# Kernel tuning notes

Hardware: AMD Instinct MI355X
Metric: run time of the kernel (lower is better)

The kernel has to match this reference:

```python
import jax, jax.numpy as jnp
import numpy as np

N_NODES = 10000
N_EDGES = 320000
NODE_F = 64
EDGE_F = 32
H = 256
L = 6
HEADS = 8
OUT = H // HEADS
N_GRAPHS = 16
NEG_SLOPE = 0.2  # PyG GATConv leaky_relu slope


def setup_inputs() -> dict:
    key = jax.random.key(0)
    ks = jax.random.split(key, 32)
    s = 0.05
    f32 = jnp.float32
    inp = {}
    inp["x"] = jax.random.normal(ks[0], (N_NODES, NODE_F), f32)
    inp["edge_index"] = jax.random.randint(ks[1], (2, N_EDGES), 0, N_NODES)
    inp["edge_attr"] = jax.random.normal(ks[2], (N_EDGES, EDGE_F), f32)
    inp["batch"] = jnp.sort(jax.random.randint(ks[3], (N_NODES,), 0, N_GRAPHS))
    # embeddings
    inp["node_w"] = jax.random.normal(ks[4], (H, NODE_F), f32) * s
    inp["node_b"] = jnp.zeros((H,), f32)
    inp["edge_emb_w"] = jax.random.normal(ks[5], (H, EDGE_F), f32) * s
    inp["edge_emb_b"] = jnp.zeros((H,), f32)
    # stacked GATConv params (shared lin for src/dst since in_channels is int)
    inp["lin_w"] = jax.random.normal(ks[6], (L, H, H), f32) * s
    inp["att_src"] = jax.random.normal(ks[7], (L, HEADS, OUT), f32) * s
    inp["att_dst"] = jax.random.normal(ks[8], (L, HEADS, OUT), f32) * s
    inp["att_edge"] = jax.random.normal(ks[9], (L, HEADS, OUT), f32) * s
    inp["lin_edge_w"] = jax.random.normal(ks[10], (L, H, H), f32) * s
    inp["conv_b"] = jnp.zeros((L, H), f32)
    inp["ln_g"] = jnp.ones((L, H), f32)
    inp["ln_b"] = jnp.zeros((L, H), f32)
    # MLP heads: Linear(2H->H), Linear(H->H/2), Linear(H/2->3)
    inp["pw1"] = jax.random.normal(ks[11], (H, 2 * H), f32) * s
    inp["pb1"] = jnp.zeros((H,), f32)
    inp["pw2"] = jax.random.normal(ks[12], (H // 2, H), f32) * s
    inp["pb2"] = jnp.zeros((H // 2,), f32)
    inp["pw3"] = jax.random.normal(ks[13], (3, H // 2), f32) * s
    inp["pb3"] = jnp.zeros((3,), f32)
    inp["mw1"] = jax.random.normal(ks[14], (H, 2 * H), f32) * s
    inp["mb1"] = jnp.zeros((H,), f32)
    inp["mw2"] = jax.random.normal(ks[15], (H // 2, H), f32) * s
    inp["mb2"] = jnp.zeros((H // 2,), f32)
    inp["mw3"] = jax.random.normal(ks[16], (3, H // 2), f32) * s
    inp["mb3"] = jnp.zeros((3,), f32)
    return inp


def _ln(x, g, b):
    mu = jnp.mean(x, -1, keepdims=True)
    var = jnp.mean(jnp.square(x - mu), -1, keepdims=True)
    return g * (x - mu) * jax.lax.rsqrt(var + 1e-5) + b


def _mlp(z, w1, b1, w2, b2, w3, b3):
    h = jax.nn.gelu(z @ w1.T + b1, approximate=False)
    h = jax.nn.gelu(h @ w2.T + b2, approximate=False)
    return jax.nn.sigmoid(h @ w3.T + b3)


def _gnn_forward(x, edge_attr, src, dst, batch,
                 node_w, node_b, edge_emb_w, edge_emb_b,
                 lin_w, att_src, att_dst, att_edge, lin_edge_w, conv_b,
                 ln_g, ln_b,
                 pw1, pb1, pw2, pb2, pw3, pb3,
                 mw1, mb1, mw2, mb2, mw3, mb3):
    h = x @ node_w.T + node_b                       # [N, H]
    ea = edge_attr @ edge_emb_w.T + edge_emb_b      # [E, H]
    # PyG add_self_loops(fill_value='mean'): loop attr = mean of incoming edge attrs
    cnt = jax.ops.segment_sum(jnp.ones((N_EDGES,), h.dtype), dst, N_NODES)
    loop_attr = jax.ops.segment_sum(ea, dst, N_NODES) / jnp.maximum(cnt, 1.0)[:, None]
    ea_full = jnp.concatenate([ea, loop_attr], 0)   # [E+N, H]
    loops = jnp.arange(N_NODES, dtype=src.dtype)
    src_f = jnp.concatenate([src, loops])
    dst_f = jnp.concatenate([dst, loops])
    for i in range(L):
        x_in = h
        xw = (h @ lin_w[i].T).reshape(N_NODES, HEADS, OUT)
        eap = (ea_full @ lin_edge_w[i].T).reshape(-1, HEADS, OUT)
        a_src = jnp.sum(xw * att_src[i], -1)        # [N, heads]
        a_dst = jnp.sum(xw * att_dst[i], -1)
        alpha = a_src[src_f] + a_dst[dst_f] + jnp.sum(eap * att_edge[i], -1)  # [E+N, heads]
        alpha = jnp.where(alpha > 0, alpha, NEG_SLOPE * alpha)
        amax = jax.ops.segment_max(alpha, dst_f, N_NODES)
        e = jnp.exp(alpha - amax[dst_f])
        denom = jax.ops.segment_sum(e, dst_f, N_NODES)
        w = e / (denom[dst_f] + 1e-16)
        msg = xw[src_f] * w[:, :, None]             # [E+N, heads, out]
        hi = jax.ops.segment_sum(msg, dst_f, N_NODES).reshape(N_NODES, H) + conv_b[i]
        hi = jax.nn.gelu(_ln(hi, ln_g[i], ln_b[i]), approximate=False)
        h = hi + x_in if i > 0 else hi
    sums = jax.ops.segment_sum(h, batch, N_GRAPHS)  # [G, H]
    ncnt = jax.ops.segment_sum(jnp.ones((N_NODES,), h.dtype), batch, N_GRAPHS)
    mean = sums / jnp.maximum(ncnt, 1.0)[:, None]
    xg = jnp.concatenate([mean, sums], 1)           # [G, 2H]
    params = _mlp(xg, pw1, pb1, pw2, pb2, pw3, pb3)
    metrics = _mlp(xg, mw1, mb1, mw2, mb2, mw3, mb3)
    return params, metrics


def reference(x, edge_index, edge_attr, batch,
              node_w, node_b, edge_emb_w, edge_emb_b,
              lin_w, att_src, att_dst, att_edge, lin_edge_w, conv_b,
              ln_g, ln_b,
              pw1, pb1, pw2, pb2, pw3, pb3,
              mw1, mb1, mw2, mb2, mw3, mb3):
    return _gnn_forward(x, edge_attr, edge_index[0], edge_index[1], batch,
                        node_w, node_b, edge_emb_w, edge_emb_b,
                        lin_w, att_src, att_dst, att_edge, lin_edge_w, conv_b,
                        ln_g, ln_b,
                        pw1, pb1, pw2, pb2, pw3, pb3,
                        mw1, mb1, mw2, mb2, mw3, mb3)
```

## Files before the change

### kernel.cpp

```cpp
#include <hip/hip_runtime.h>
#include <math.h>

#define NN 10000
#define NE 320000
#define NODE_F 64
#define EDGE_F 32
#define HDIM 256
#define HEADS 8
#define LAYERS 6
#define NG 16
#define NPB 2
#define NOUT 48
#define LOG2E 1.4426950408889634f

typedef __attribute__((ext_vector_type(8))) short short8;
typedef __attribute__((ext_vector_type(4))) float float4v;
typedef __attribute__((ext_vector_type(2))) float floatx2;

__global__ void count_kernel(const int* __restrict__ dst, int* __restrict__ cnt) {
    int e = blockIdx.x * 256 + threadIdx.x;
    if (e < NE) atomicAdd(&cnt[dst[e]], 1);
}

__global__ void scan_kernel(const int* __restrict__ cnt, int* __restrict__ row_ptr,
                            int* __restrict__ pos) {
    __shared__ int wsum[16];
    __shared__ int woff[16];
    int t = threadIdx.x;
    int lane = t & 63, wid = t >> 6;
    const int chunk = 10;
    int lo = t * chunk;
    int loc[10];
    int s = 0;
    #pragma unroll
    for (int k = 0; k < 10; ++k) {
        int i = lo + k;
        int v = (i < NN) ? cnt[i] : 0;
        loc[k] = v;
        s += v;
    }
    int inc = s;
    #pragma unroll
    for (int off = 1; off < 64; off <<= 1) {
        int v = __shfl_up(inc, off, 64);
        if (lane >= off) inc += v;
    }
    if (lane == 63) wsum[wid] = inc;
    __syncthreads();
    if (t < 16) {
        int inc2 = wsum[t];
        #pragma unroll
        for (int off = 1; off < 16; off <<= 1) {
            int u = __shfl_up(inc2, off, 16);
            if (t >= off) inc2 += u;
        }
        woff[t] = inc2;
    }
    __syncthreads();
    int base = inc - s + (wid ? woff[wid - 1] : 0);
    #pragma unroll
    for (int k = 0; k < 10; ++k) {
        int i = lo + k;
        if (i < NN) {
            row_ptr[i] = base;
            pos[i] = base;
            base += loc[k];
        }
    }
    if (t == 1023) row_ptr[NN] = woff[15];
}

__device__ __forceinline__ ushort f2bf(float f) {
    union { float f; unsigned u; } v; v.f = f;
    unsigned u = v.u;
    return (ushort)((u + 0x7fffu + ((u >> 16) & 1u)) >> 16);
}
__device__ __forceinline__ float bf2f(ushort b) {
    union { unsigned u; float f; } v; v.u = ((unsigned)b) << 16; return v.f;
}

__global__ __launch_bounds__(256) void prep_kernel(const float* __restrict__ att_edge,
                                                   const float* __restrict__ lin_edge_w,
                                                   const float* __restrict__ eew,
                                                   const float* __restrict__ eeb,
                                                   ushort* __restrict__ webbf,
                                                   float* __restrict__ bebuf) {
    int ih = blockIdx.x;
    int i = ih >> 3, h = ih & 7;
    __shared__ float vsh[HDIM];
    int t = threadIdx.x;
    float s = 0.f;
    const float* ae = att_edge + ih * 32;
    const float* lw = lin_edge_w + ((size_t)i * HDIM + h * 32) * HDIM + t;
    #pragma unroll
    for (int o = 0; o < 32; ++o) s += ae[o] * lw[(size_t)o * HDIM];
    vsh[t] = s;
    __syncthreads();
    if (t < EDGE_F) {
        float acc = 0.f;
        for (int k = 0; k < HDIM; ++k) acc += vsh[k] * eew[k * EDGE_F + t];
        webbf[ih * EDGE_F + t] = f2bf(acc * LOG2E);
    } else if (t == EDGE_F) {
        float acc = 0.f;
        for (int k = 0; k < HDIM; ++k) acc += vsh[k] * eeb[k];
        bebuf[ih] = acc * LOG2E;
    }
}

__global__ __launch_bounds__(256) void scatterE_kernel(const int* __restrict__ src,
                                                       const int* __restrict__ dst,
                                                       const float* __restrict__ edge_attr,
                                                       int* __restrict__ pos,
                                                       int* __restrict__ csr_src,
                                                       const ushort* __restrict__ web,
                                                       const float* __restrict__ be,
                                                       ushort* __restrict__ preEb) {
    int wv = threadIdx.x >> 6, l = threadIdx.x & 63;
    int base = blockIdx.x * 64 + wv * 16;
    int m = l & 15, kq = (l >> 4) * 8;
    int idxl = 0;
    if (l < 16) {
        int e = base + l;
        int d = dst[e];
        idxl = atomicAdd(&pos[d], 1);
        csr_src[idxl] = src[e];
    }
    const float* ar = edge_attr + (size_t)(base + m) * EDGE_F + kq;
    float4 a0 = *(const float4*)(ar);
    float4 a1 = *(const float4*)(ar + 4);
    short8 afrag;
    afrag[0] = (short)f2bf(a0.x); afrag[1] = (short)f2bf(a0.y);
    afrag[2] = (short)f2bf(a0.z); afrag[3] = (short)f2bf(a0.w);
    afrag[4] = (short)f2bf(a1.x); afrag[5] = (short)f2bf(a1.y);
    afrag[6] = (short)f2bf(a1.z); afrag[7] = (short)f2bf(a1.w);
    float4v zero = {0.f, 0.f, 0.f, 0.f};
    float4v acc[3];
    #pragma unroll
    for (int ct = 0; ct < 3; ++ct) {
        short8 bfrag = *(const short8*)(web + (size_t)(ct * 16 + m) * EDGE_F + kq);
        acc[ct] = __builtin_amdgcn_mfma_f32_16x16x32_bf16(afrag, bfrag, zero, 0, 0, 0);
    }
    #pragma unroll
    for (int ct = 0; ct < 3; ++ct) {
        int oc = ct * 16 + m;
        int li = oc >> 3, hh = oc & 7;
        float bv = be[oc];
        #pragma unroll
        for (int r = 0; r < 4; ++r) {
            int row = (l >> 4) * 4 + r;
            int ridx = __shfl(idxl, row, 64);
            preEb[(size_t)li * NE * 8 + (size_t)ridx * 8 + hh] = f2bf(acc[ct][r] + bv);
        }
    }
}

__global__ __launch_bounds__(256) void preL_kernel(const ushort* __restrict__ preEb,
                                                   const int* __restrict__ row_ptr,
                                                   float* __restrict__ preL) {
    int g = threadIdx.x >> 5, c = threadIdx.x & 31;
    int n = blockIdx.x * 8 + g;
    int start = row_ptr[n], end = row_ptr[n + 1];
    int deg = end - start;
    float s[NOUT] = {};
    for (int idx = start + c; idx < end; idx += 32) {
        #pragma unroll
        for (int li = 0; li < LAYERS; ++li) {
            uint4 pk = *(const uint4*)(preEb + (size_t)li * NE * 8 + (size_t)idx * 8);
            s[li * 8 + 0] += bf2f((ushort)(pk.x & 0xffff));
            s[li * 8 + 1] += bf2f((ushort)(pk.x >> 16));
            s[li * 8 + 2] += bf2f((ushort)(pk.y & 0xffff));
            s[li * 8 + 3] += bf2f((ushort)(pk.y >> 16));
            s[li * 8 + 4] += bf2f((ushort)(pk.z & 0xffff));
            s[li * 8 + 5] += bf2f((ushort)(pk.z >> 16));
            s[li * 8 + 6] += bf2f((ushort)(pk.w & 0xffff));
            s[li * 8 + 7] += bf2f((ushort)(pk.w >> 16));
        }
    }
    #pragma unroll
    for (int off = 16; off >= 1; off >>= 1)
        #pragma unroll
        for (int h = 0; h < NOUT; ++h) s[h] += __shfl_xor(s[h], off, 32);
    if (c == 0) {
        float invd = deg > 0 ? 1.f / (float)deg : 0.f;
        for (int li = 0; li < LAYERS; ++li) {
            float4* dstp = (float4*)(preL + ((size_t)li * NN + n) * 8);
            dstp[0] = make_float4(s[li * 8 + 0] * invd, s[li * 8 + 1] * invd,
                                  s[li * 8 + 2] * invd, s[li * 8 + 3] * invd);
            dstp[1] = make_float4(s[li * 8 + 4] * invd, s[li * 8 + 5] * invd,
                                  s[li * 8 + 6] * invd, s[li * 8 + 7] * invd);
        }
    }
}

__global__ void tobf_all_kernel(const float* __restrict__ lin_w, const float* __restrict__ node_w,
                                const float* __restrict__ x, ushort* __restrict__ wbhi,
                                ushort* __restrict__ nwhi, ushort* __restrict__ xhi) {
    const int N1 = LAYERS * HDIM * HDIM;
    const int N2 = N1 + HDIM * NODE_F;
    const int N3 = N2 + NN * NODE_F;
    int i = blockIdx.x * 256 + threadIdx.x;
    if (i < N1) wbhi[i] = f2bf(lin_w[i]);
    else if (i < N2) nwhi[i - N1] = f2bf(node_w[i - N1]);
    else if (i < N3) xhi[i - N2] = f2bf(x[i - N2]);
}

__global__ __launch_bounds__(128) void gemm_bf1(const ushort* __restrict__ Ah,
                                                const ushort* __restrict__ Bh,
                                                const float* __restrict__ bias,
                                                float* __restrict__ C,
                                                ushort* __restrict__ Chi,
                                                unsigned char* __restrict__ Cf8,
                                                const float* __restrict__ att_s,
                                                const float* __restrict__ att_d,
                                                float* __restrict__ a_src,
                                                float* __restrict__ a_dst,
                                                int N, int K, int J) {
    __shared__ ushort sAh[64][40], sBh[64][40];
    int nb = blockIdx.y * 64, jb = blockIdx.x * 64;
    int t = threadIdx.x, w = t >> 6, l = t & 63;
    int srow = t >> 1, sq = (t & 1) * 16;
    int fr = l & 15, fq = (l >> 4) * 8;
    float4v acc[2][4] = {};
    for (int kt = 0; kt < K; kt += 32) {
        int gr = nb + srow;
        short8 a0 = {0,0,0,0,0,0,0,0}, a1 = {0,0,0,0,0,0,0,0};
        if (gr < N) {
            const short8* pa = (const short8*)(Ah + (size_t)gr * K + kt + sq);
            a0 = pa[0]; a1 = pa[1];
        }
        *(short8*)&sAh[srow][sq] = a0; *(short8*)&sAh[srow][sq + 8] = a1;
        const short8* pb = (const short8*)(Bh + (size_t)(jb + srow) * K + kt + sq);
        short8 b0 = pb[0], b1 = pb[1];
        *(short8*)&sBh[srow][sq] = b0; *(short8*)&sBh[srow][sq + 8] = b1;
        __syncthreads();
        short8 bh[4];
        #pragma unroll
        for (int nt = 0; nt < 4; ++nt)
            bh[nt] = *(const short8*)&sBh[nt * 16 + fr][fq];
        #pragma unroll
        for (int mt = 0; mt < 2; ++mt) {
            short8 ah = *(const short8*)&sAh[w * 32 + mt * 16 + fr][fq];
            #pragma unroll
            for (int nt = 0; nt < 4; ++nt)
                acc[mt][nt] = __builtin_amdgcn_mfma_f32_16x16x32_bf16(ah, bh[nt], acc[mt][nt], 0, 0, 0);
        }
        __syncthreads();
    }
    #pragma unroll
    for (int mt = 0; mt < 2; ++mt) {
        #pragma unroll
        for (int nt = 0; nt < 4; ++nt) {
            int col = jb + nt * 16 + fr;
            float bv = bias ? bias[col] : 0.f;
            #pragma unroll
            for (int r = 0; r < 4; ++r) {
                int row = nb + w * 32 + mt * 16 + (l >> 4) * 4 + r;
                if (row < N) {
                    float v = acc[mt][nt][r] + bv;
                    if (C) C[(size_t)row * J + col] = v;
                    if (Chi) Chi[(size_t)row * J + col] = f2bf(v);
                    if (Cf8) {
                        int pk8 = __builtin_amdgcn_cvt_pk_fp8_f32(v, v, 0, false);
                        Cf8[(size_t)row * J + col] = (unsigned char)(pk8 & 0xff);
                    }
                }
            }
        }
    }
    if (att_s) {
        int head0 = jb >> 5;
        float cs[4], cd[4];
        #pragma unroll
        for (int nt = 0; nt < 4; ++nt) {
            cs[nt] = att_s[jb + nt * 16 + fr] * LOG2E;
            cd[nt] = att_d[jb + nt * 16 + fr] * LOG2E;
        }
        #pragma unroll
        for (int mt = 0; mt < 2; ++mt) {
            #pragma unroll
            for (int r = 0; r < 4; ++r) {
                float s0 = acc[mt][0][r] * cs[0] + acc[mt][1][r] * cs[1];
                float s1 = acc[mt][2][r] * cs[2] + acc[mt][3][r] * cs[3];
                float d0 = acc[mt][0][r] * cd[0] + acc[mt][1][r] * cd[1];
                float d1 = acc[mt][2][r] * cd[2] + acc[mt][3][r] * cd[3];
                #pragma unroll
                for (int off = 8; off >= 1; off >>= 1) {
                    s0 += __shfl_xor(s0, off, 16);
                    s1 += __shfl_xor(s1, off, 16);
                    d0 += __shfl_xor(d0, off, 16);
                    d1 += __shfl_xor(d1, off, 16);
                }
                if (fr == 0) {
                    int row = nb + w * 32 + mt * 16 + (l >> 4) * 4 + r;
                    if (row < N) {
                        a_src[row * 8 + head0]     = s0;
                        a_src[row * 8 + head0 + 1] = s1;
                        a_dst[row * 8 + head0]     = d0;
                        a_dst[row * 8 + head0 + 1] = d1;
                    }
                }
            }
        }
    }
}

__device__ __forceinline__ float gelu_exact(float x) {
    return 0.5f * x * (1.f + erff(x * 0.70710678118654752f));
}

__global__ __launch_bounds__(64 * NPB) void node_kernel(const unsigned char* __restrict__ xwf8,
                                                  const ushort* __restrict__ pb,
                                                  const float* __restrict__ preL,
                                                  const float* __restrict__ a_src,
                                                  const float* __restrict__ a_dst,
                                                  const int* __restrict__ row_ptr,
                                                  const int* __restrict__ csr_src,
                                                  const float* __restrict__ h_prev,
                                                  float* __restrict__ h_next,
                                                  ushort* __restrict__ hhi,
                                                  const float* __restrict__ cb,
                                                  const float* __restrict__ lg,
                                                  const float* __restrict__ lb, int first) {
    int wv = threadIdx.x >> 6, l = threadIdx.x & 63;
    int n = blockIdx.x * NPB + wv;
    int start = row_ptr[n], end = row_ptr[n + 1];
    int hc = l >> 3;
    int hc8 = l & 56;
    int jj = l & 7;
    float adnh = a_dst[n * 8 + hc];
    const unsigned char* xb = xwf8 + 4 * l;

    float den, acc[4];
    {
        float al = a_src[n * 8 + hc] + adnh + preL[n * 8 + hc];
        al = fminf(fmaxf(al, 0.2f * al), 57.7f);
        float wself = exp2f(al);
        den = wself;
        unsigned gs = *(const unsigned*)(xb + (size_t)n * HDIM);
        floatx2 lo = __builtin_amdgcn_cvt_pk_f32_fp8(gs, false);
        floatx2 hi = __builtin_amdgcn_cvt_pk_f32_fp8(gs, true);
        acc[0] = wself * lo.x;
        acc[1] = wself * lo.y;
        acc[2] = wself * hi.x;
        acc[3] = wself * hi.y;
    }
    int idx = start;
    for (; idx + 8 <= end; idx += 8) {
        int sn[8];
        #pragma unroll
        for (int j = 0; j < 8; ++j) sn[j] = csr_src[idx + j];
        int sn_t = csr_src[idx + jj];
        float p_t = bf2f(pb[(size_t)(idx + jj) * 8 + hc]);
        float a_t = a_src[(size_t)sn_t * 8 + hc] + adnh + p_t;
        float w_t = exp2f(fminf(fmaxf(a_t, 0.2f * a_t), 57.7f));
        unsigned g[8];
        #pragma unroll
        for (int j = 0; j < 8; ++j) g[j] = *(const unsigned*)(xb + (size_t)sn[j] * HDIM);
        #pragma unroll
        for (int j = 0; j < 8; ++j) {
            float wj = __shfl(w_t, hc8 + j, 64);
            floatx2 lo = __builtin_amdgcn_cvt_pk_f32_fp8(g[j], false);
            floatx2 hi = __builtin_amdgcn_cvt_pk_f32_fp8(g[j], true);
            den += wj;
            acc[0] += wj * lo.x;
            acc[1] += wj * lo.y;
            acc[2] += wj * hi.x;
            acc[3] += wj * hi.y;
        }
    }
    for (; idx < end; ++idx) {
        int sn = csr_src[idx];
        unsigned g = *(const unsigned*)(xb + (size_t)sn * HDIM);
        float a = a_src[(size_t)sn * 8 + hc] + adnh + bf2f(pb[(size_t)idx * 8 + hc]);
        float wt = exp2f(fminf(fmaxf(a, 0.2f * a), 57.7f));
        floatx2 lo = __builtin_amdgcn_cvt_pk_f32_fp8(g, false);
        floatx2 hi = __builtin_amdgcn_cvt_pk_f32_fp8(g, true);
        den += wt;
        acc[0] += wt * lo.x;
        acc[1] += wt * lo.y;
        acc[2] += wt * hi.x;
        acc[3] += wt * hi.y;
    }
    float4 cb4 = *(const float4*)(cb + 4 * l);
    float invh = 1.f / (den + 1e-16f);
    acc[0] = acc[0] * invh + cb4.x;
    acc[1] = acc[1] * invh + cb4.y;
    acc[2] = acc[2] * invh + cb4.z;
    acc[3] = acc[3] * invh + cb4.w;

    float part = acc[0] + acc[1] + acc[2] + acc[3];
    #pragma unroll
    for (int off = 32; off >= 1; off >>= 1) part += __shfl_xor(part, off, 64);
    float mu = part * (1.f / 256.f);
    float p2 = 0.f;
    #pragma unroll
    for (int j = 0; j < 4; ++j) {
        float d = acc[j] - mu;
        p2 += d * d;
    }
    #pragma unroll
    for (int off = 32; off >= 1; off >>= 1) p2 += __shfl_xor(p2, off, 64);
    float rstd = rsqrtf(p2 * (1.f / 256.f) + 1e-5f);

    float4 lg4 = *(const float4*)(lg + 4 * l);
    float4 lb4 = *(const float4*)(lb + 4 * l);
    float o4[4];
    float lgv[4] = {lg4.x, lg4.y, lg4.z, lg4.w};
    float lbv[4] = {lb4.x, lb4.y, lb4.z, lb4.w};
    float4 hp = make_float4(0.f, 0.f, 0.f, 0.f);
    if (!first) hp = *(const float4*)(h_prev + (size_t)n * HDIM + 4 * l);
    float hpv[4] = {hp.x, hp.y, hp.z, hp.w};
    #pragma unroll
    for (int j = 0; j < 4; ++j) {
        float y = (acc[j] - mu) * rstd * lgv[j] + lbv[j];
        o4[j] = gelu_exact(y) + hpv[j];
    }
    *(float4*)(h_next + (size_t)n * HDIM + 4 * l) = make_float4(o4[0], o4[1], o4[2], o4[3]);
    if (hhi) {
        uint2 ph;
        ph.x = (unsigned)f2bf(o4[0]) | ((unsigned)f2bf(o4[1]) << 16);
        ph.y = (unsigned)f2bf(o4[2]) | ((unsigned)f2bf(o4[3]) << 16);
        *(uint2*)(hhi + (size_t)n * HDIM + 4 * l) = ph;
    }
}

__global__ __launch_bounds__(256) void graph_sum_kernel(const float* __restrict__ h,
                                                        const int* __restrict__ batch,
                                                        float* __restrict__ sums) {
    int t = threadIdx.x;
    int n0 = blockIdx.x * 64;
    int n1 = min(NN, n0 + 64);
    float acc = 0.f;
    int cur = batch[n0];
    for (int n = n0; n < n1; ++n) {
        int b = batch[n];
        if (b != cur) {
            atomicAdd(&sums[cur * HDIM + t], acc);
            acc = 0.f;
            cur = b;
        }
        acc += h[(size_t)n * HDIM + t];
    }
    atomicAdd(&sums[cur * HDIM + t], acc);
}

__device__ __forceinline__ int lower_bound_dev(const int* a, int n, int v) {
    int lo = 0, hi = n;
    while (lo < hi) {
        int mid = (lo + hi) >> 1;
        if (a[mid] < v) lo = mid + 1; else hi = mid;
    }
    return lo;
}

__global__ __launch_bounds__(256) void mlp_kernel(const float* __restrict__ sums,
                                                  const int* __restrict__ batch,
                                                  const float* __restrict__ pw1,
                                                  const float* __restrict__ pb1,
                                                  const float* __restrict__ pw2,
                                                  const float* __restrict__ pb2,
                                                  const float* __restrict__ pw3,
                                                  const float* __restrict__ pb3,
                                                  const float* __restrict__ mw1,
                                                  const float* __restrict__ mb1,
                                                  const float* __restrict__ mw2,
                                                  const float* __restrict__ mb2,
                                                  const float* __restrict__ mw3,
                                                  const float* __restrict__ mb3,
                                                  float* __restrict__ out) {
    int g = blockIdx.x, which = blockIdx.y;
    const float* w1 = which ? mw1 : pw1; const float* b1 = which ? mb1 : pb1;
    const float* w2 = which ? mw2 : pw2; const float* b2 = which ? mb2 : pb2;
    const float* w3 = which ? mw3 : pw3; const float* b3 = which ? mb3 : pb3;
    __shared__ float xg[512];
    __shared__ float h1[256];
    __shared__ float h2[128];
    __shared__ float cinv_s;
    int t = threadIdx.x;
    if (t == 0) {
        int s0 = lower_bound_dev(batch, NN, g), s1 = lower_bound_dev(batch, NN, g + 1);
        cinv_s = 1.f / fmaxf((float)(s1 - s0), 1.f);
    }
    __syncthreads();
    float sv = sums[g * HDIM + t];
    xg[t] = sv * cinv_s;
    xg[256 + t] = sv;
    __syncthreads();
    {
        const float* wr = w1 + (size_t)t * 512;
        float acc = 0.f;
        #pragma unroll 8
        for (int k = 0; k < 512; k += 4) {
            float4 wv = *(const float4*)(wr + k);
            acc += wv.x * xg[k] + wv.y * xg[k + 1] + wv.z * xg[k + 2] + wv.w * xg[k + 3];
        }
        h1[t] = gelu_exact(acc + b1[t]);
    }
    __syncthreads();
    {
        int row = t >> 1, hf = t & 1;
        const float* wr = w2 + (size_t)row * 256 + hf * 128;
        const float* hx = h1 + hf * 128;
        float acc = 0.f;
        #pragma unroll 8
        for (int k = 0; k < 128; k += 4) {
            float4 wv = *(const float4*)(wr + k);
            acc += wv.x * hx[k] + wv.y * hx[k + 1] + wv.z * hx[k + 2] + wv.w * hx[k + 3];
        }
        acc += __shfl_xor(acc, 1, 64);
        if (hf == 0) h2[row] = gelu_exact(acc + b2[row]);
    }
    __syncthreads();
    if (t < 64) {
        float v0 = h2[t], v1 = h2[64 + t];
        #pragma unroll
        for (int o = 0; o < 3; ++o) {
            float p = w3[o * 128 + t] * v0 + w3[o * 128 + 64 + t] * v1;
            #pragma unroll
            for (int off = 32; off >= 1; off >>= 1) p += __shfl_xor(p, off, 64);
            if (t == 0) out[which * (NG * 3) + g * 3 + o] = 1.f / (1.f + expf(-(p + b3[o])));
        }
    }
}

extern "C" void kernel_launch(void* const* d_in, const int* in_sizes, int n_in, void* d_out,
                              int out_size, void* d_ws, size_t ws_size, hipStream_t stream) {
    const float* x         = (const float*)d_in[0];
    const int*   ei        = (const int*)d_in[1];
    const int*   src       = ei;
    const int*   dst       = ei + NE;
    const float* edge_attr = (const float*)d_in[2];
    const int*   batch     = (const int*)d_in[3];
    const float* node_w    = (const float*)d_in[4];
    const float* node_b    = (const float*)d_in[5];
    const float* eew       = (const float*)d_in[6];
    const float* eeb       = (const float*)d_in[7];
    const float* lin_w     = (const float*)d_in[8];
    const float* att_src   = (const float*)d_in[9];
    const float* att_dst   = (const float*)d_in[10];
    const float* att_edge  = (const float*)d_in[11];
    const float* lin_edge_w= (const float*)d_in[12];
    const float* conv_b    = (const float*)d_in[13];
    const float* ln_g      = (const float*)d_in[14];
    const float* ln_b      = (const float*)d_in[15];
    const float* pw1 = (const float*)d_in[16]; const float* pb1 = (const float*)d_in[17];
    const float* pw2 = (const float*)d_in[18]; const float* pb2 = (const float*)d_in[19];
    const float* pw3 = (const float*)d_in[20]; const float* pb3 = (const float*)d_in[21];
    const float* mw1 = (const float*)d_in[22]; const float* mb1 = (const float*)d_in[23];
    const float* mw2 = (const float*)d_in[24]; const float* mb2 = (const float*)d_in[25];
    const float* mw3 = (const float*)d_in[26]; const float* mb3 = (const float*)d_in[27];
    float* out = (float*)d_out;

    float* wsf = (float*)d_ws;
    float* hA        = wsf; wsf += (size_t)NN * HDIM;
    float* hB        = wsf; wsf += (size_t)NN * HDIM;
    float* preL      = wsf; wsf += (size_t)LAYERS * NN * 8;
    float* a_src     = wsf; wsf += (size_t)NN * HEADS;
    float* a_dst     = wsf; wsf += (size_t)NN * HEADS;
    float* bebuf     = wsf; wsf += 64;
    ushort* ubuf = (ushort*)wsf;
    ushort* preEb = ubuf; ubuf += (size_t)NE * NOUT;
    ushort* webbf = ubuf; ubuf += (size_t)NOUT * EDGE_F;
    ushort* hhi  = ubuf; ubuf += (size_t)NN * HDIM;
    unsigned char* xwf8 = (unsigned char*)ubuf; ubuf += (size_t)NN * HDIM / 2;
    ushort* wbhi = ubuf; ubuf += (size_t)LAYERS * HDIM * HDIM;
    ushort* xhi  = ubuf; ubuf += (size_t)NN * NODE_F;
    ushort* nwhi = ubuf; ubuf += (size_t)HDIM * NODE_F;
    int* ibuf    = (int*)ubuf;
    int* cnt     = ibuf; ibuf += NN + 16;
    float* sums  = (float*)ibuf; ibuf += NG * HDIM;
    int* row_ptr = ibuf; ibuf += NN + 16;
    int* pos     = ibuf; ibuf += NN + 16;
    int* csr_src = ibuf; ibuf += NE;

    hipMemsetAsync(cnt, 0, (NN + 16 + NG * HDIM) * sizeof(int), stream);
    count_kernel<<<(NE + 255) / 256, 256, 0, stream>>>(dst, cnt);
    scan_kernel<<<1, 1024, 0, stream>>>(cnt, row_ptr, pos);

    prep_kernel<<<LAYERS * HEADS, 256, 0, stream>>>(att_edge, lin_edge_w, eew, eeb, webbf, bebuf);
    scatterE_kernel<<<NE / 64, 256, 0, stream>>>(src, dst, edge_attr, pos, csr_src,
                                                 webbf, bebuf, preEb);
    preL_kernel<<<NN / 8, 256, 0, stream>>>(preEb, row_ptr, preL);

    {
        const int total = LAYERS * HDIM * HDIM + HDIM * NODE_F + NN * NODE_F;
        tobf_all_kernel<<<(total + 255) / 256, 256, 0, stream>>>(lin_w, node_w, x,
                                                                 wbhi, nwhi, xhi);
    }

    {
        dim3 grid(HDIM / 64, (NN + 63) / 64);
        gemm_bf1<<<grid, 128, 0, stream>>>(xhi, nwhi, node_b, nullptr, hhi, nullptr,
                                           nullptr, nullptr, nullptr, nullptr,
                                           NN, NODE_F, HDIM);
    }

    float* cur = hA;
    float* nxt = hB;
    for (int i = 0; i < LAYERS; ++i) {
        dim3 grid(HDIM / 64, (NN + 63) / 64);
        gemm_bf1<<<grid, 128, 0, stream>>>(hhi, wbhi + (size_t)i * HDIM * HDIM, nullptr,
                                           nullptr, nullptr, xwf8,
                                           att_src + i * HEADS * 32, att_dst + i * HEADS * 32,
                                           a_src, a_dst, NN, HDIM, HDIM);
        node_kernel<<<NN / NPB, 64 * NPB, 0, stream>>>(
            xwf8, preEb + (size_t)i * NE * 8, preL + (size_t)i * NN * 8, a_src, a_dst,
            row_ptr, csr_src, cur, nxt, (i == LAYERS - 1) ? nullptr : hhi,
            conv_b + i * HDIM, ln_g + i * HDIM, ln_b + i * HDIM, i == 0 ? 1 : 0);
        float* tmp = cur; cur = nxt; nxt = tmp;
    }

    graph_sum_kernel<<<(NN + 63) / 64, 256, 0, stream>>>(cur, batch, sums);
    {
        dim3 gm(NG, 2);
        mlp_kernel<<<gm, 256, 0, stream>>>(sums, batch, pw1, pb1, pw2, pb2, pw3, pb3,
                                           mw1, mb1, mw2, mb2, mw3, mb3, out);
    }
}
```

Baseline: 524.4 us.

## Store edge logits in original order and fold self-loop mean into node kernel

The edge-logit GEMM now writes preEb in original edge order. A separate scatter kernel builds a CSR of (src, edge id) pairs. The preL pre-pass is removed: node_kernel sums the edge logits while aggregating and computes the self-loop mean logit at the end. This drops one full pass over the 6-layer edge buffer and the preL storage, at the cost of non-contiguous gathers of preEb through edge ids in every layer and an extra scatter kernel.

```diff
diff --git a/kernel.cpp b/kernel.cpp
--- a/kernel.cpp
+++ b/kernel.cpp
@@ -68,6 +68,15 @@
         }
     }
     if (t == 1023) row_ptr[NN] = woff[15];
+}
+
+__global__ void scatter_kernel(const int* __restrict__ src, const int* __restrict__ dst,
+                               int* __restrict__ pos, int2* __restrict__ csr_se) {
+    int e = blockIdx.x * 256 + threadIdx.x;
+    if (e >= NE) return;
+    int d = dst[e];
+    int idx = atomicAdd(&pos[d], 1);
+    csr_se[idx] = make_int2(src[e], e);
 }
 
 __device__ __forceinline__ ushort f2bf(float f) {
@@ -107,24 +116,13 @@
     }
 }
 
-__global__ __launch_bounds__(256) void scatterE_kernel(const int* __restrict__ src,
-                                                       const int* __restrict__ dst,
-                                                       const float* __restrict__ edge_attr,
-                                                       int* __restrict__ pos,
-                                                       int* __restrict__ csr_src,
-                                                       const ushort* __restrict__ web,
-                                                       const float* __restrict__ be,
-                                                       ushort* __restrict__ preEb) {
+__global__ __launch_bounds__(256) void preE_kernel(const float* __restrict__ edge_attr,
+                                                   const ushort* __restrict__ web,
+                                                   const float* __restrict__ be,
+                                                   ushort* __restrict__ preEb) {
     int wv = threadIdx.x >> 6, l = threadIdx.x & 63;
     int base = blockIdx.x * 64 + wv * 16;
     int m = l & 15, kq = (l >> 4) * 8;
-    int idxl = 0;
-    if (l < 16) {
-        int e = base + l;
-        int d = dst[e];
-        idxl = atomicAdd(&pos[d], 1);
-        csr_src[idxl] = src[e];
-    }
     const float* ar = edge_attr + (size_t)(base + m) * EDGE_F + kq;
     float4 a0 = *(const float4*)(ar);
     float4 a1 = *(const float4*)(ar + 4);
@@ -148,46 +146,7 @@
         #pragma unroll
         for (int r = 0; r < 4; ++r) {
             int row = (l >> 4) * 4 + r;
-            int ridx = __shfl(idxl, row, 64);
-            preEb[(size_t)li * NE * 8 + (size_t)ridx * 8 + hh] = f2bf(acc[ct][r] + bv);
-        }
-    }
-}
-
-__global__ __launch_bounds__(256) void preL_kernel(const ushort* __restrict__ preEb,
-                                                   const int* __restrict__ row_ptr,
-                                                   float* __restrict__ preL) {
-    int g = threadIdx.x >> 5, c = threadIdx.x & 31;
-    int n = blockIdx.x * 8 + g;
-    int start = row_ptr[n], end = row_ptr[n + 1];
-    int deg = end - start;
-    float s[NOUT] = {};
-    for (int idx = start + c; idx < end; idx += 32) {
-        #pragma unroll
-        for (int li = 0; li < LAYERS; ++li) {
-            uint4 pk = *(const uint4*)(preEb + (size_t)li * NE * 8 + (size_t)idx * 8);
-            s[li * 8 + 0] += bf2f((ushort)(pk.x & 0xffff));
-            s[li * 8 + 1] += bf2f((ushort)(pk.x >> 16));
-            s[li * 8 + 2] += bf2f((ushort)(pk.y & 0xffff));
-            s[li * 8 + 3] += bf2f((ushort)(pk.y >> 16));
-            s[li * 8 + 4] += bf2f((ushort)(pk.z & 0xffff));
-            s[li * 8 + 5] += bf2f((ushort)(pk.z >> 16));
-            s[li * 8 + 6] += bf2f((ushort)(pk.w & 0xffff));
-            s[li * 8 + 7] += bf2f((ushort)(pk.w >> 16));
-        }
-    }
-    #pragma unroll
-    for (int off = 16; off >= 1; off >>= 1)
-        #pragma unroll
-        for (int h = 0; h < NOUT; ++h) s[h] += __shfl_xor(s[h], off, 32);
-    if (c == 0) {
-        float invd = deg > 0 ? 1.f / (float)deg : 0.f;
-        for (int li = 0; li < LAYERS; ++li) {
-            float4* dstp = (float4*)(preL + ((size_t)li * NN + n) * 8);
-            dstp[0] = make_float4(s[li * 8 + 0] * invd, s[li * 8 + 1] * invd,
-                                  s[li * 8 + 2] * invd, s[li * 8 + 3] * invd);
-            dstp[1] = make_float4(s[li * 8 + 4] * invd, s[li * 8 + 5] * invd,
-                                  s[li * 8 + 6] * invd, s[li * 8 + 7] * invd);
+            preEb[(size_t)li * NE * 8 + (size_t)(base + row) * 8 + hh] = f2bf(acc[ct][r] + bv);
         }
     }
 }
@@ -310,11 +269,10 @@
 
 __global__ __launch_bounds__(64 * NPB) void node_kernel(const unsigned char* __restrict__ xwf8,
                                                   const ushort* __restrict__ pb,
-                                                  const float* __restrict__ preL,
                                                   const float* __restrict__ a_src,
                                                   const float* __restrict__ a_dst,
                                                   const int* __restrict__ row_ptr,
-                                                  const int* __restrict__ csr_src,
+                                                  const int2* __restrict__ csr_se,
                                                   const float* __restrict__ h_prev,
                                                   float* __restrict__ h_next,
                                                   ushort* __restrict__ hhi,
@@ -330,32 +288,25 @@
     float adnh = a_dst[n * 8 + hc];
     const unsigned char* xb = xwf8 + 4 * l;
 
-    float den, acc[4];
-    {
-        float al = a_src[n * 8 + hc] + adnh + preL[n * 8 + hc];
-        al = fminf(fmaxf(al, 0.2f * al), 57.7f);
-        float wself = exp2f(al);
-        den = wself;
-        unsigned gs = *(const unsigned*)(xb + (size_t)n * HDIM);
-        floatx2 lo = __builtin_amdgcn_cvt_pk_f32_fp8(gs, false);
-        floatx2 hi = __builtin_amdgcn_cvt_pk_f32_fp8(gs, true);
-        acc[0] = wself * lo.x;
-        acc[1] = wself * lo.y;
-        acc[2] = wself * hi.x;
-        acc[3] = wself * hi.y;
-    }
-    int idx = start;
-    for (; idx + 8 <= end; idx += 8) {
-        int sn[8];
-        #pragma unroll
-        for (int j = 0; j < 8; ++j) sn[j] = csr_src[idx + j];
-        int sn_t = csr_src[idx + jj];
-        float p_t = bf2f(pb[(size_t)(idx + jj) * 8 + hc]);
-        float a_t = a_src[(size_t)sn_t * 8 + hc] + adnh + p_t;
-        float w_t = exp2f(fminf(fmaxf(a_t, 0.2f * a_t), 57.7f));
+    float den = 0.f, acc[4] = {0.f, 0.f, 0.f, 0.f};
+    float psum = 0.f;
+    for (int idx = start; idx < end; idx += 8) {
+        int myi = idx + jj;
+        bool valid = myi < end;
+        int2 se = valid ? csr_se[myi] : make_int2(n, 0);
+        int snj[8];
+        #pragma unroll
+        for (int j = 0; j < 8; ++j) snj[j] = __shfl(se.x, hc8 + j, 64);
         unsigned g[8];
         #pragma unroll
-        for (int j = 0; j < 8; ++j) g[j] = *(const unsigned*)(xb + (size_t)sn[j] * HDIM);
+        for (int j = 0; j < 8; ++j) g[j] = *(const unsigned*)(xb + (size_t)snj[j] * HDIM);
+        float w_t = 0.f;
+        if (valid) {
+            float p_t = bf2f(pb[(size_t)se.y * 8 + hc]);
+            float a_t = a_src[(size_t)se.x * 8 + hc] + adnh + p_t;
+            w_t = exp2f(fminf(fmaxf(a_t, 0.2f * a_t), 57.7f));
+            psum += p_t;
+        }
         #pragma unroll
         for (int j = 0; j < 8; ++j) {
             float wj = __shfl(w_t, hc8 + j, 64);
@@ -368,18 +319,22 @@
             acc[3] += wj * hi.y;
         }
     }
-    for (; idx < end; ++idx) {
-        int sn = csr_src[idx];
-        unsigned g = *(const unsigned*)(xb + (size_t)sn * HDIM);
-        float a = a_src[(size_t)sn * 8 + hc] + adnh + bf2f(pb[(size_t)idx * 8 + hc]);
-        float wt = exp2f(fminf(fmaxf(a, 0.2f * a), 57.7f));
-        floatx2 lo = __builtin_amdgcn_cvt_pk_f32_fp8(g, false);
-        floatx2 hi = __builtin_amdgcn_cvt_pk_f32_fp8(g, true);
-        den += wt;
-        acc[0] += wt * lo.x;
-        acc[1] += wt * lo.y;
-        acc[2] += wt * hi.x;
-        acc[3] += wt * hi.y;
+    #pragma unroll
+    for (int off = 1; off < 8; off <<= 1) psum += __shfl_xor(psum, off, 64);
+    int deg = end - start;
+    float preLv = deg > 0 ? psum / (float)deg : 0.f;
+    {
+        float al = a_src[n * 8 + hc] + adnh + preLv;
+        al = fminf(fmaxf(al, 0.2f * al), 57.7f);
+        float wself = exp2f(al);
+        den += wself;
+        unsigned gs = *(const unsigned*)(xb + (size_t)n * HDIM);
+        floatx2 lo = __builtin_amdgcn_cvt_pk_f32_fp8(gs, false);
+        floatx2 hi = __builtin_amdgcn_cvt_pk_f32_fp8(gs, true);
+        acc[0] += wself * lo.x;
+        acc[1] += wself * lo.y;
+        acc[2] += wself * hi.x;
+        acc[3] += wself * hi.y;
     }
     float4 cb4 = *(const float4*)(cb + 4 * l);
     float invh = 1.f / (den + 1e-16f);
@@ -554,7 +509,6 @@
     float* wsf = (float*)d_ws;
     float* hA        = wsf; wsf += (size_t)NN * HDIM;
     float* hB        = wsf; wsf += (size_t)NN * HDIM;
-    float* preL      = wsf; wsf += (size_t)LAYERS * NN * 8;
     float* a_src     = wsf; wsf += (size_t)NN * HEADS;
     float* a_dst     = wsf; wsf += (size_t)NN * HEADS;
     float* bebuf     = wsf; wsf += 64;
@@ -571,16 +525,16 @@
     float* sums  = (float*)ibuf; ibuf += NG * HDIM;
     int* row_ptr = ibuf; ibuf += NN + 16;
     int* pos     = ibuf; ibuf += NN + 16;
-    int* csr_src = ibuf; ibuf += NE;
+    ibuf += (((size_t)ibuf & 4) ? 1 : 0);
+    int2* csr_se = (int2*)ibuf; ibuf += 2 * NE;
 
     hipMemsetAsync(cnt, 0, (NN + 16 + NG * HDIM) * sizeof(int), stream);
     count_kernel<<<(NE + 255) / 256, 256, 0, stream>>>(dst, cnt);
     scan_kernel<<<1, 1024, 0, stream>>>(cnt, row_ptr, pos);
+    scatter_kernel<<<(NE + 255) / 256, 256, 0, stream>>>(src, dst, pos, csr_se);
 
     prep_kernel<<<LAYERS * HEADS, 256, 0, stream>>>(att_edge, lin_edge_w, eew, eeb, webbf, bebuf);
-    scatterE_kernel<<<NE / 64, 256, 0, stream>>>(src, dst, edge_attr, pos, csr_src,
-                                                 webbf, bebuf, preEb);
-    preL_kernel<<<NN / 8, 256, 0, stream>>>(preEb, row_ptr, preL);
+    preE_kernel<<<NE / 64, 256, 0, stream>>>(edge_attr, webbf, bebuf, preEb);
 
     {
         const int total = LAYERS * HDIM * HDIM + HDIM * NODE_F + NN * NODE_F;
@@ -604,8 +558,8 @@
                                            att_src + i * HEADS * 32, att_dst + i * HEADS * 32,
                                            a_src, a_dst, NN, HDIM, HDIM);
         node_kernel<<<NN / NPB, 64 * NPB, 0, stream>>>(
-            xwf8, preEb + (size_t)i * NE * 8, preL + (size_t)i * NN * 8, a_src, a_dst,
-            row_ptr, csr_src, cur, nxt, (i == LAYERS - 1) ? nullptr : hhi,
+            xwf8, preEb + (size_t)i * NE * 8, a_src, a_dst,
+            row_ptr, csr_se, cur, nxt, (i == LAYERS - 1) ? nullptr : hhi,
             conv_b + i * HDIM, ln_g + i * HDIM, ln_b + i * HDIM, i == 0 ? 1 : 0);
         float* tmp = cur; cur = nxt; nxt = tmp;
     }
```

Result: faster. 509.1 us (-2.9%).
